# Performance work log

Hardware: AMD Instinct MI355X
Metric: run time of the kernel (lower is better)

The kernel has to match this reference:

```python
import jax, jax.numpy as jnp
import numpy as np
from math import sqrt

B, N, CS, H, D, K = 8, 256, 512, 8, 64, 32
NB = 2 * K + 1          # no_bins = 65
CT = 2048               # c_transition
INF = 1e9
WL = sqrt(0.5)          # w_L
EPS = 1e-5


def setup_inputs() -> dict:
    key = jax.random.key(0)
    ks = jax.random.split(key, 10)
    sc = 0.02
    return {
        "s": jax.random.normal(ks[0], (B, N, CS), jnp.float32),
        "masks": jnp.ones((B, N), jnp.bool_),
        "wq": jax.random.normal(ks[1], (CS, D * H), jnp.float32) * sc,
        "wk": jax.random.normal(ks[2], (CS, D * H), jnp.float32) * sc,
        "wv": jax.random.normal(ks[3], (CS, D * H), jnp.float32) * sc,
        "wb": jax.random.normal(ks[4], (NB, H), jnp.float32) * sc,
        "wo": jax.random.normal(ks[5], ((NB + D) * H, CS), jnp.float32) * sc,
        "bo": jnp.zeros((CS,), jnp.float32),
        "ln1_g": jnp.ones((CS,), jnp.float32),
        "ln1_b": jnp.zeros((CS,), jnp.float32),
        "w1": jax.random.normal(ks[6], (CS, CT), jnp.float32) * sc,
        "b1": jnp.zeros((CT,), jnp.float32),
        "w2": jax.random.normal(ks[7], (CT, CS), jnp.float32) * sc,
        "b2": jnp.zeros((CS,), jnp.float32),
        "ln2_g": jnp.ones((CS,), jnp.float32),
        "ln2_b": jnp.zeros((CS,), jnp.float32),
    }


def _layernorm(x, g, b):
    m = jnp.mean(x, -1, keepdims=True)
    v = jnp.var(x, -1, keepdims=True)
    return (x - m) * jax.lax.rsqrt(v + EPS) * g + b


def _heads(x):  # [B,N,D*H] -> [B,H,N,D]  (torch: reshape(B,N,D,H) then move H forward)
    return jnp.transpose(x.reshape(B, N, D, H), (0, 3, 1, 2))


def reference(s, masks, wq, wk, wv, wb, wo, bo, ln1_g, ln1_b, w1, b1, w2, b2, ln2_g, ln2_b):
    mf = masks.astype(s.dtype)                       # [B,N]
    sq = mf[:, :, None] * mf[:, None, :]             # [B,N,N]

    # relative position one-hot, clipped to [-K, K] -> [N,N,NB]
    r = jnp.arange(N)
    dmat = jnp.clip(r[:, None] - r[None, :], -K, K) + K
    relpos_base = jax.nn.one_hot(dmat, NB, dtype=s.dtype)
    relpos = relpos_base[None] * sq[..., None]       # [B,N,N,NB]

    b_bias = jnp.einsum('bijc,ch->bhij', relpos, wb)  # [B,H,N,N]

    q = _heads(s @ wq)                               # [B,H,N,D]
    k = _heads(s @ wk)
    v = _heads(s @ wv)

    logits = WL * (jnp.einsum('bhid,bhjd->bhij', q, k) / sqrt(D) + b_bias)
    logits = logits - INF * (1.0 - sq)[:, None]      # mask
    a = jax.nn.softmax(logits, axis=-1)              # [B,H,N,N]

    # pairwise aggregation and value aggregation (einsum avoids [B,H,N,N,NB] blowup)
    o_pair = jnp.einsum('bhij,bijc->bhic', a, relpos)  # [B,H,N,NB]
    o = jnp.einsum('bhij,bhjd->bhid', a, v)            # [B,H,N,D]

    op = jnp.transpose(o_pair, (0, 2, 1, 3)).reshape(B, N, H * NB)
    ov = jnp.transpose(o, (0, 2, 1, 3)).reshape(B, N, H * D)
    embd = jnp.concatenate([op, ov], axis=-1) @ wo + bo   # [B,N,CS]

    x = _layernorm(s + embd, ln1_g, ln1_b)
    ff = jax.nn.relu(x @ w1 + b1) @ w2 + b2
    x = _layernorm(x + ff, ln2_g, ln2_b)
    return x, a
```

## Files before the change

kernel.cpp:

```cpp
#include <hip/hip_runtime.h>
#include <hip/hip_bf16.h>
#include <cstdint>

#define B_ 8
#define N_ 256
#define CS_ 512
#define H_ 8
#define D_ 64
#define K_ 32
#define NB_ 65
#define CT_ 2048
#define WL_ 0.70710678118654752f

typedef __attribute__((ext_vector_type(8))) short bf16x8;
typedef __attribute__((ext_vector_type(4))) float f32x4;

#define GLOBAL_AS __attribute__((address_space(1)))
#define LDS_AS __attribute__((address_space(3)))

__device__ __forceinline__ void async16(void* lds, const void* g) {
  __builtin_amdgcn_global_load_lds((const GLOBAL_AS uint32_t*)g,
                                   (LDS_AS uint32_t*)lds, 16, 0, 0);
}

__device__ __forceinline__ ushort f2bf(float v) {
  __hip_bfloat16 hb = __float2bfloat16(v);
  return *(ushort*)&hb;
}

__device__ __forceinline__ float bf2f(ushort u) {
  union { uint32_t ui; float f; } cv; cv.ui = (uint32_t)u << 16;
  return cv.f;
}

__global__ __launch_bounds__(128, 2) void gemm_bf16(
    const ushort* __restrict__ A, const ushort* __restrict__ Bt,
    const float* __restrict__ bias, float* __restrict__ C,
    ushort* __restrict__ Cb, int M, int Nc, int Kd, int flags) {
  __shared__ ushort As[2][64 * 64];
  __shared__ ushort Bs[2][64 * 64];
  int tid = threadIdx.x;
  int bm = blockIdx.y * 64, bn = blockIdx.x * 64;
  int S = gridDim.z, z = blockIdx.z;
  int T = Kd >> 6;
  int it0 = (z * T) / S, it1 = ((z + 1) * T) / S;
  if (flags & 8)  C  += (size_t)z * M * Nc;
  if (flags & 32) Cb += (size_t)z * M * Nc;
  int w = tid >> 6, l = tid & 63;
  int lm = l & 15, lq = l >> 4;
  int srow = tid >> 3;
  int sg = tid & 7;

  f32x4 acc[2][4];
#pragma unroll
  for (int i = 0; i < 2; ++i)
#pragma unroll
    for (int j = 0; j < 4; ++j) acc[i][j] = (f32x4){0.f, 0.f, 0.f, 0.f};

  {
    int k0 = it0 << 6;
#pragma unroll
    for (int r = 0; r < 4; ++r) {
      int row = r * 16 + srow;
      int gl = sg ^ (row & 7);
      async16(&As[0][row * 64 + sg * 8],
              A + (size_t)(bm + row) * Kd + k0 + gl * 8);
      async16(&Bs[0][row * 64 + sg * 8],
              Bt + (size_t)(bn + row) * Kd + k0 + gl * 8);
    }
  }
  for (int it = it0; it < it1; ++it) {
    int cur = (it - it0) & 1;
    __syncthreads();
    if (it + 1 < it1) {
      int nxt = cur ^ 1;
      int k0 = (it + 1) << 6;
#pragma unroll
      for (int r = 0; r < 4; ++r) {
        int row = r * 16 + srow;
        int gl = sg ^ (row & 7);
        async16(&As[nxt][row * 64 + sg * 8],
                A + (size_t)(bm + row) * Kd + k0 + gl * 8);
        async16(&Bs[nxt][row * 64 + sg * 8],
                Bt + (size_t)(bn + row) * Kd + k0 + gl * 8);
      }
    }
#pragma unroll
    for (int kk = 0; kk < 2; ++kk) {
      bf16x8 af[2], bfr[4];
#pragma unroll
      for (int i = 0; i < 2; ++i) {
        int ma = w * 32 + 16 * i + lm;
        af[i] = *(const bf16x8*)&As[cur][ma * 64 + ((kk * 4 + lq) ^ (ma & 7)) * 8];
      }
#pragma unroll
      for (int j = 0; j < 4; ++j) {
        int nb = 16 * j + lm;
        bfr[j] = *(const bf16x8*)&Bs[cur][nb * 64 + ((kk * 4 + lq) ^ (nb & 7)) * 8];
      }
#pragma unroll
      for (int i = 0; i < 2; ++i)
#pragma unroll
        for (int j = 0; j < 4; ++j)
          acc[i][j] = __builtin_amdgcn_mfma_f32_16x16x32_bf16(
              af[i], bfr[j], acc[i][j], 0, 0, 0);
    }
  }
  __syncthreads();

  int lr = l >> 3, lc = l & 7;
  ushort* Tb = &As[0][0] + w * 2048;

  if (flags & 16) {
    int which = bn >> 9;
    int hh = (bn & 511) >> 6;
    int b = bm >> 8, nn0 = bm & 255;
    if (which == 2) {
#pragma unroll
      for (int j = 0; j < 4; ++j)
#pragma unroll
        for (int i = 0; i < 2; ++i) {
          ushort pk[4];
#pragma unroll
          for (int r = 0; r < 4; ++r) pk[r] = f2bf(acc[i][j][r]);
          *(uint2*)&Tb[(16 * j + lm) * 32 + 16 * i + lq * 4] = *(uint2*)pk;
        }
    } else {
#pragma unroll
      for (int j = 0; j < 4; ++j)
#pragma unroll
        for (int i = 0; i < 2; ++i)
#pragma unroll
          for (int r = 0; r < 4; ++r)
            Tb[(16 * i + lq * 4 + r) * 64 + 16 * j + lm] = f2bf(acc[i][j][r]);
    }
    __asm__ __volatile__("" ::: "memory");
    ushort* dstb = Cb + (size_t)which * 1048576 + (size_t)(b * 8 + hh) * 16384;
    if (which == 2) {
      int vr = l >> 2, vc = l & 3;
#pragma unroll
      for (int p = 0; p < 4; ++p) {
        int rowL = p * 16 + vr;
        bf16x8 vv = *(const bf16x8*)&Tb[rowL * 32 + vc * 8];
        *(bf16x8*)(dstb + (size_t)rowL * 256 + nn0 + w * 32 + vc * 8) = vv;
      }
    } else {
#pragma unroll
      for (int p = 0; p < 4; ++p) {
        int rowL = p * 8 + lr;
        bf16x8 vv = *(const bf16x8*)&Tb[rowL * 64 + lc * 8];
        *(bf16x8*)(dstb + (size_t)(nn0 + w * 32 + rowL) * 64 + lc * 8) = vv;
      }
    }
    return;
  }
  if (flags & 4) {
#pragma unroll
    for (int j = 0; j < 4; ++j) {
      float bv = ((flags & 1) && z == 0) ? bias[bn + 16 * j + lm] : 0.f;
#pragma unroll
      for (int i = 0; i < 2; ++i)
#pragma unroll
        for (int r = 0; r < 4; ++r) {
          float v = acc[i][j][r] + bv;
          if (flags & 2) v = fmaxf(v, 0.f);
          Tb[(16 * i + lq * 4 + r) * 64 + 16 * j + lm] = f2bf(v);
        }
    }
    __asm__ __volatile__("" ::: "memory");
#pragma unroll
    for (int p = 0; p < 4; ++p) {
      int rowL = p * 8 + lr;
      bf16x8 vv = *(const bf16x8*)&Tb[rowL * 64 + lc * 8];
      *(bf16x8*)(Cb + (size_t)(bm + w * 32 + rowL) * Nc + bn + lc * 8) = vv;
    }
    return;
  }
#pragma unroll
  for (int j = 0; j < 4; ++j) {
    int col = bn + 16 * j + lm;
    float bv = ((flags & 1) && z == 0) ? bias[col] : 0.f;
#pragma unroll
    for (int i = 0; i < 2; ++i)
#pragma unroll
      for (int r = 0; r < 4; ++r) {
        int row = bm + w * 32 + 16 * i + lq * 4 + r;
        float v = acc[i][j][r] + bv;
        if (flags & 2) v = fmaxf(v, 0.f);
        C[(size_t)row * Nc + col] = v;
      }
  }
}

__global__ __launch_bounds__(256) void prep_all(
    const float* __restrict__ s, __hip_bfloat16* __restrict__ s_bf,
    const float* __restrict__ wq, const float* __restrict__ wk,
    const float* __restrict__ wv, const float* __restrict__ wo,
    const float* __restrict__ w1, const float* __restrict__ w2,
    __hip_bfloat16* __restrict__ wqkvT, __hip_bfloat16* __restrict__ wopT,
    __hip_bfloat16* __restrict__ w1T, __hip_bfloat16* __restrict__ w2T) {
  int blk = blockIdx.x;
  if (blk < 512) {
    int i = blk * 256 + threadIdx.x;
    float4 a = ((const float4*)s)[i * 2];
    float4 c = ((const float4*)s)[i * 2 + 1];
    ushort pk[8] = {f2bf(a.x), f2bf(a.y), f2bf(a.z), f2bf(a.w),
                    f2bf(c.x), f2bf(c.y), f2bf(c.z), f2bf(c.w)};
    *(uint4*)&((ushort*)s_bf)[i * 8] = *(uint4*)pk;
    return;
  }
  blk -= 512;
  __shared__ float tile[32][33];
  const float* src;
  __hip_bfloat16* dst;
  int R, C, Kpad, tX, tIdx, whichBase = -1;
  if (blk < 768) {
    int zz = blk >> 8; tIdx = blk & 255;
    src = zz == 0 ? wq : zz == 1 ? wk : wv;
    dst = wqkvT; whichBase = zz * 512; R = 512; C = 512; Kpad = 512; tX = 16;
  } else if (blk < 1312) {
    tIdx = blk - 768; src = wo; dst = wopT; R = 1032; C = 512; Kpad = 1088; tX = 16;
  } else if (blk < 2336) {
    tIdx = blk - 1312; src = w1; dst = w1T; R = 512; C = 2048; Kpad = 512; tX = 64;
  } else {
    tIdx = blk - 2336; src = w2; dst = w2T; R = 2048; C = 512; Kpad = 2048; tX = 16;
  }
  int c0 = (tIdx % tX) * 32, r0 = (tIdx / tX) * 32;
  int tx = threadIdx.x & 31, ty = threadIdx.x >> 5;
#pragma unroll
  for (int yy = 0; yy < 32; yy += 8) {
    int r = r0 + ty + yy, c = c0 + tx;
    tile[ty + yy][tx] = (r < R && c < C) ? src[(size_t)r * C + c] : 0.f;
  }
  __syncthreads();
#pragma unroll
  for (int yy = 0; yy < 32; yy += 8) {
    int cc = c0 + ty + yy, k = r0 + tx;
    if (cc < C && k < Kpad) {
      int n = (whichBase >= 0) ? (whichBase + (cc & 7) * 64 + (cc >> 3)) : cc;
      dst[(size_t)n * Kpad + k] = __float2bfloat16(tile[tx][ty + yy]);
    }
  }
}

__global__ __launch_bounds__(128) void attn_fused(
    const ushort* __restrict__ qh, const ushort* __restrict__ kh,
    const ushort* __restrict__ vT, const int* __restrict__ masks,
    const float* __restrict__ wb, float* __restrict__ a_out,
    ushort* __restrict__ cat) {
  int strip = blockIdx.x & 7, bh = blockIdx.x >> 3;
  int h = bh & 7, b = bh >> 3;
  __shared__ ushort Ks[256 * 64];
  __shared__ ushort Ps[32 * 64];
  __shared__ float wbs[NB_];
  __shared__ float mfj[256];
  int tid = threadIdx.x;
  int srow = tid >> 3, sg = tid & 7;
#pragma unroll
  for (int rr = 0; rr < 16; ++rr) {
    int row = rr * 16 + srow;
    int gl = sg ^ (row & 7);
    async16(&Ks[row * 64 + sg * 8],
            kh + ((size_t)bh * 256 + row) * 64 + gl * 8);
  }
  int w = tid >> 6, l = tid & 63, lm = l & 15, lq = l >> 4;
  bf16x8 qf[2];
  {
    const ushort* qrow =
        qh + ((size_t)bh * 256 + strip * 32 + w * 16 + lm) * 64 + lq * 8;
    qf[0] = *(const bf16x8*)qrow;
    qf[1] = *(const bf16x8*)(qrow + 32);
  }
  if (tid < NB_) wbs[tid] = wb[tid * H_ + h];
  mfj[tid]       = (masks[b * 256 + tid] != 0) ? 1.f : 0.f;
  mfj[tid + 128] = (masks[b * 256 + tid + 128] != 0) ? 1.f : 0.f;
  __syncthreads();

  f32x4 acc[16];
#pragma unroll
  for (int ct = 0; ct < 16; ++ct) {
    int krow = ct * 16 + lm;
    bf16x8 kf0 = *(const bf16x8*)&Ks[krow * 64 + ((lq) ^ (krow & 7)) * 8];
    bf16x8 kf1 = *(const bf16x8*)&Ks[krow * 64 + ((4 + lq) ^ (krow & 7)) * 8];
    f32x4 zf = (f32x4){0.f, 0.f, 0.f, 0.f};
    zf = __builtin_amdgcn_mfma_f32_16x16x32_bf16(qf[0], kf0, zf, 0, 0, 0);
    acc[ct] = __builtin_amdgcn_mfma_f32_16x16x32_bf16(qf[1], kf1, zf, 0, 0, 0);
  }
  int ibase = strip * 32 + w * 16 + lq * 4;
  float mfi[4];
#pragma unroll
  for (int r = 0; r < 4; ++r) mfi[r] = mfj[ibase + r];
#pragma unroll
  for (int ct = 0; ct < 16; ++ct) {
    int j = ct * 16 + lm;
    float mj = mfj[j];
#pragma unroll
    for (int r = 0; r < 4; ++r) {
      int i = ibase + r;
      int diff = i - j;
      int cb = diff < -K_ ? 0 : (diff > K_ ? 2 * K_ : diff + K_);
      float sq = mfi[r] * mj;
      acc[ct][r] = WL_ * (acc[ct][r] * 0.125f + wbs[cb] * sq) - 1e9f * (1.f - sq);
    }
  }
  float mx[4], sm[4];
#pragma unroll
  for (int r = 0; r < 4; ++r) {
    float m = acc[0][r];
#pragma unroll
    for (int ct = 1; ct < 16; ++ct) m = fmaxf(m, acc[ct][r]);
#pragma unroll
    for (int o = 1; o < 16; o <<= 1) m = fmaxf(m, __shfl_xor(m, o, 64));
    mx[r] = m;
  }
#pragma unroll
  for (int ct = 0; ct < 16; ++ct)
#pragma unroll
    for (int r = 0; r < 4; ++r) acc[ct][r] = __expf(acc[ct][r] - mx[r]);
#pragma unroll
  for (int r = 0; r < 4; ++r) {
    float s = 0.f;
#pragma unroll
    for (int ct = 0; ct < 16; ++ct) s += acc[ct][r];
#pragma unroll
    for (int o = 1; o < 16; o <<= 1) s += __shfl_xor(s, o, 64);
    sm[r] = 1.f / s;
  }
  float p0[4] = {0.f, 0.f, 0.f, 0.f}, p64[4] = {0.f, 0.f, 0.f, 0.f};
#pragma unroll
  for (int ct = 0; ct < 16; ++ct) {
    int j = ct * 16 + lm;
    float mj = mfj[j];
#pragma unroll
    for (int r = 0; r < 4; ++r) {
      int i = ibase + r;
      float aval = acc[ct][r] * sm[r];
      a_out[((size_t)bh * 256 + i) * 256 + j] = aval;
      float val = aval * mfi[r] * mj;
      int diff = i - j;
      if (diff <= -K_)      p0[r] += val;
      else if (diff >= K_)  p64[r] += val;
      else cat[((size_t)(b * 256 + i)) * 1088 + h * 65 + diff + K_] = f2bf(val);
    }
  }
#pragma unroll
  for (int r = 0; r < 4; ++r)
#pragma unroll
    for (int o = 1; o < 16; o <<= 1) {
      p0[r]  += __shfl_xor(p0[r], o, 64);
      p64[r] += __shfl_xor(p64[r], o, 64);
    }
  if (lm == 0) {
#pragma unroll
    for (int r = 0; r < 4; ++r) {
      int i = ibase + r;
      cat[((size_t)(b * 256 + i)) * 1088 + h * 65 + 0]      = f2bf(p0[r]);
      cat[((size_t)(b * 256 + i)) * 1088 + h * 65 + 2 * K_] = f2bf(p64[r]);
    }
  }
#pragma unroll
  for (int r = 0; r < 4; ++r) {
    int i = ibase + r;
#pragma unroll
    for (int t = 0; t < 4; ++t) {
      int c = 1 + lm + 16 * t;
      if (c < 64) {
        int j = i - c + K_;
        if (j < 0 || j > 255)
          cat[((size_t)(b * 256 + i)) * 1088 + h * 65 + c] = 0;
      }
    }
  }
  if (h == 0) {
    for (int idx = tid; idx < 32 * 56; idx += 128) {
      int r = idx / 56, c = 1032 + (idx - r * 56);
      cat[((size_t)(b * 256 + strip * 32 + r)) * 1088 + c] = 0;
    }
  }
  f32x4 acc2[4];
#pragma unroll
  for (int nt = 0; nt < 4; ++nt) acc2[nt] = (f32x4){0.f, 0.f, 0.f, 0.f};
  const ushort* vbase = vT + (size_t)bh * 16384;
#pragma unroll
  for (int qt = 0; qt < 4; ++qt) {
    bf16x8 vf0[4], vf1[4];
#pragma unroll
    for (int nt = 0; nt < 4; ++nt) {
      const ushort* vrow = vbase + (size_t)(nt * 16 + lm) * 256 + qt * 64 + lq * 8;
      vf0[nt] = *(const bf16x8*)vrow;
      vf1[nt] = *(const bf16x8*)(vrow + 32);
    }
#pragma unroll
    for (int ctl = 0; ctl < 4; ++ctl) {
      int ct = qt * 4 + ctl;
#pragma unroll
      for (int r = 0; r < 4; ++r) {
        int rowl = w * 16 + lq * 4 + r;
        int g = ctl * 2 + (lm >> 3);
        Ps[rowl * 64 + ((g ^ (rowl & 7)) << 3) + (lm & 7)] =
            f2bf(acc[ct][r] * sm[r]);
      }
    }
    int prow = w * 16 + lm;
#pragma unroll
    for (int kst = 0; kst < 2; ++kst) {
      bf16x8 af = *(const bf16x8*)&Ps[prow * 64 + (((kst * 4 + lq) ^ (prow & 7)) << 3)];
#pragma unroll
      for (int nt = 0; nt < 4; ++nt)
        acc2[nt] = __builtin_amdgcn_mfma_f32_16x16x32_bf16(
            af, kst ? vf1[nt] : vf0[nt], acc2[nt], 0, 0, 0);
    }
  }
#pragma unroll
  for (int nt = 0; nt < 4; ++nt) {
    int d = nt * 16 + lm;
#pragma unroll
    for (int r = 0; r < 4; ++r) {
      int i = ibase + r;
      cat[((size_t)(b * 256 + i)) * 1088 + 520 + h * 64 + d] = f2bf(acc2[nt][r]);
    }
  }
}

__global__ __launch_bounds__(128) void ln_sum(
    const float* __restrict__ x1, const ushort* __restrict__ xp,
    int S, int stride, const float* __restrict__ g,
    const float* __restrict__ bta, float* __restrict__ out,
    __hip_bfloat16* __restrict__ out_bf) {
  __shared__ float redA[2], redB[2];
  int row = blockIdx.x, tid = threadIdx.x;
  size_t base = (size_t)row * 512;
  float4 v = *(const float4*)(x1 + base + tid * 4);
  for (int s = 0; s < S; ++s) {
    uint2 p = *(const uint2*)(xp + (size_t)s * stride + base + tid * 4);
    v.x += bf2f((ushort)(p.x & 0xffff));
    v.y += bf2f((ushort)(p.x >> 16));
    v.z += bf2f((ushort)(p.y & 0xffff));
    v.w += bf2f((ushort)(p.y >> 16));
  }
  float su = v.x + v.y + v.z + v.w;
  float sq = v.x * v.x + v.y * v.y + v.z * v.z + v.w * v.w;
#pragma unroll
  for (int o = 32; o > 0; o >>= 1) {
    su += __shfl_xor(su, o, 64);
    sq += __shfl_xor(sq, o, 64);
  }
  int w = tid >> 6;
  if ((tid & 63) == 0) { redA[w] = su; redB[w] = sq; }
  __syncthreads();
  su = redA[0] + redA[1]; sq = redB[0] + redB[1];
  float mean = su * (1.f / 512.f);
  float var = sq * (1.f / 512.f) - mean * mean;
  float inv = rsqrtf(var + 1e-5f);
  float4 gv = *(const float4*)(g + tid * 4);
  float4 bv = *(const float4*)(bta + tid * 4);
  float4 o4;
  o4.x = (v.x - mean) * inv * gv.x + bv.x;
  o4.y = (v.y - mean) * inv * gv.y + bv.y;
  o4.z = (v.z - mean) * inv * gv.z + bv.z;
  o4.w = (v.w - mean) * inv * gv.w + bv.w;
  *(float4*)(out + base + tid * 4) = o4;
  if (out_bf) {
    ushort pk[4] = {f2bf(o4.x), f2bf(o4.y), f2bf(o4.z), f2bf(o4.w)};
    *(uint2*)&((ushort*)out_bf)[base + tid * 4] = *(uint2*)pk;
  }
}

extern "C" void kernel_launch(void* const* d_in, const int* in_sizes, int n_in,
                              void* d_out, int out_size, void* d_ws, size_t ws_size,
                              hipStream_t stream) {
  const float* s     = (const float*)d_in[0];
  const int*   masks = (const int*)d_in[1];
  const float* wq = (const float*)d_in[2];
  const float* wk = (const float*)d_in[3];
  const float* wv = (const float*)d_in[4];
  const float* wb = (const float*)d_in[5];
  const float* wo = (const float*)d_in[6];
  const float* bo = (const float*)d_in[7];
  const float* ln1_g = (const float*)d_in[8];
  const float* ln1_b = (const float*)d_in[9];
  const float* w1 = (const float*)d_in[10];
  const float* b1 = (const float*)d_in[11];
  const float* w2 = (const float*)d_in[12];
  const float* b2 = (const float*)d_in[13];
  const float* ln2_g = (const float*)d_in[14];
  const float* ln2_b = (const float*)d_in[15];

  float* out_x = (float*)d_out;
  float* out_a = out_x + 1048576;

  float* ws = (float*)d_ws;
  ushort* embd_part = (ushort*)(ws + 0);
  float* xbuf       = ws + 4194304;
  ushort* ff_part   = (ushort*)(ws + 5242880);
  ushort* qkv_bf    = (ushort*)(ws + 9437184);
  ushort* q_bf = qkv_bf;
  ushort* k_bf = qkv_bf + 1048576;
  ushort* v_bf = qkv_bf + 2097152;
  ushort* cat_bf = (ushort*)(ws + 10223616);
  __hip_bfloat16* h_bf  = (__hip_bfloat16*)(ws + 11337728);
  __hip_bfloat16* s_bf  = (__hip_bfloat16*)(ws + 13434880);
  __hip_bfloat16* x_bf  = (__hip_bfloat16*)(ws + 13959168);
  __hip_bfloat16* wqkvT = (__hip_bfloat16*)(ws + 14483456);
  __hip_bfloat16* wopT  = (__hip_bfloat16*)(ws + 14876672);
  __hip_bfloat16* w1T   = (__hip_bfloat16*)(ws + 15155200);
  __hip_bfloat16* w2T   = (__hip_bfloat16*)(ws + 15679488);

  dim3 blk(256), blkg(128);
  prep_all<<<dim3(3872), blk, 0, stream>>>(s, s_bf, wq, wk, wv, wo, w1, w2,
                                           wqkvT, wopT, w1T, w2T);
  gemm_bf16<<<dim3(24, 32, 1), blkg, 0, stream>>>(
      (const ushort*)s_bf, (const ushort*)wqkvT, nullptr, nullptr,
      qkv_bf, 2048, 1536, 512, 16);
  attn_fused<<<dim3(512), blkg, 0, stream>>>(q_bf, k_bf, v_bf, masks, wb,
                                             out_a, cat_bf);
  gemm_bf16<<<dim3(8, 32, 4), blkg, 0, stream>>>(
      cat_bf, (const ushort*)wopT, bo, nullptr, embd_part,
      2048, 512, 1088, 1 | 4 | 32);
  ln_sum<<<dim3(2048), blkg, 0, stream>>>(s, embd_part, 4, 1048576,
                                          ln1_g, ln1_b, xbuf, x_bf);
  gemm_bf16<<<dim3(32, 32, 1), blkg, 0, stream>>>(
      (const ushort*)x_bf, (const ushort*)w1T, b1, nullptr, (ushort*)h_bf,
      2048, 2048, 512, 1 | 2 | 4);
  gemm_bf16<<<dim3(8, 32, 4), blkg, 0, stream>>>(
      (const ushort*)h_bf, (const ushort*)w2T, b2, nullptr, ff_part,
      2048, 512, 2048, 1 | 4 | 32);
  ln_sum<<<dim3(2048), blkg, 0, stream>>>(xbuf, ff_part, 4, 1048576,
                                          ln2_g, ln2_b, out_x, nullptr);
}
```

Measured before the change: 172.4 us.

## Overlap wo/w1/w2 weight transposition with QKV GEMM and halve split-K

Splits the preprocessing so only s and the QKV weights are converted up front. The wo/w1/w2 transposes are folded into extra blocks of a new QKV GEMM kernel, so they run alongside the projection instead of before it. The transposes now use float4 loads and packed bf16 stores. Split-K for the output and FFN2 GEMMs drops from 4 to 2, which halves the partial buffers that ln_sum reduces but gives fewer blocks to hide latency.

```diff
diff --git a/kernel.cpp b/kernel.cpp
--- a/kernel.cpp
+++ b/kernel.cpp
@@ -44,7 +44,6 @@
   int S = gridDim.z, z = blockIdx.z;
   int T = Kd >> 6;
   int it0 = (z * T) / S, it1 = ((z + 1) * T) / S;
-  if (flags & 8)  C  += (size_t)z * M * Nc;
   if (flags & 32) Cb += (size_t)z * M * Nc;
   int w = tid >> 6, l = tid & 63;
   int lm = l & 15, lq = l >> 4;
@@ -111,94 +110,184 @@
   int lr = l >> 3, lc = l & 7;
   ushort* Tb = &As[0][0] + w * 2048;
 
-  if (flags & 16) {
-    int which = bn >> 9;
-    int hh = (bn & 511) >> 6;
-    int b = bm >> 8, nn0 = bm & 255;
-    if (which == 2) {
-#pragma unroll
-      for (int j = 0; j < 4; ++j)
-#pragma unroll
-        for (int i = 0; i < 2; ++i) {
-          ushort pk[4];
-#pragma unroll
-          for (int r = 0; r < 4; ++r) pk[r] = f2bf(acc[i][j][r]);
-          *(uint2*)&Tb[(16 * j + lm) * 32 + 16 * i + lq * 4] = *(uint2*)pk;
-        }
-    } else {
-#pragma unroll
-      for (int j = 0; j < 4; ++j)
-#pragma unroll
-        for (int i = 0; i < 2; ++i)
-#pragma unroll
-          for (int r = 0; r < 4; ++r)
-            Tb[(16 * i + lq * 4 + r) * 64 + 16 * j + lm] = f2bf(acc[i][j][r]);
-    }
-    __asm__ __volatile__("" ::: "memory");
-    ushort* dstb = Cb + (size_t)which * 1048576 + (size_t)(b * 8 + hh) * 16384;
-    if (which == 2) {
-      int vr = l >> 2, vc = l & 3;
-#pragma unroll
-      for (int p = 0; p < 4; ++p) {
-        int rowL = p * 16 + vr;
-        bf16x8 vv = *(const bf16x8*)&Tb[rowL * 32 + vc * 8];
-        *(bf16x8*)(dstb + (size_t)rowL * 256 + nn0 + w * 32 + vc * 8) = vv;
-      }
-    } else {
-#pragma unroll
-      for (int p = 0; p < 4; ++p) {
-        int rowL = p * 8 + lr;
-        bf16x8 vv = *(const bf16x8*)&Tb[rowL * 64 + lc * 8];
-        *(bf16x8*)(dstb + (size_t)(nn0 + w * 32 + rowL) * 64 + lc * 8) = vv;
-      }
+#pragma unroll
+  for (int j = 0; j < 4; ++j) {
+    float bv = ((flags & 1) && z == 0) ? bias[bn + 16 * j + lm] : 0.f;
+#pragma unroll
+    for (int i = 0; i < 2; ++i)
+#pragma unroll
+      for (int r = 0; r < 4; ++r) {
+        float v = acc[i][j][r] + bv;
+        if (flags & 2) v = fmaxf(v, 0.f);
+        Tb[(16 * i + lq * 4 + r) * 64 + 16 * j + lm] = f2bf(v);
+      }
+  }
+  __asm__ __volatile__("" ::: "memory");
+#pragma unroll
+  for (int p = 0; p < 4; ++p) {
+    int rowL = p * 8 + lr;
+    bf16x8 vv = *(const bf16x8*)&Tb[rowL * 64 + lc * 8];
+    *(bf16x8*)(Cb + (size_t)(bm + w * 32 + rowL) * Nc + bn + lc * 8) = vv;
+  }
+}
+
+__global__ __launch_bounds__(128, 2) void qkvT(
+    const ushort* __restrict__ A, const ushort* __restrict__ Bt,
+    ushort* __restrict__ Cb,
+    const float* __restrict__ wo, const float* __restrict__ w1,
+    const float* __restrict__ w2, ushort* __restrict__ wopT,
+    ushort* __restrict__ w1T, ushort* __restrict__ w2T) {
+  __shared__ __align__(16) ushort As[2][64 * 64];
+  __shared__ ushort Bs[2][64 * 64];
+  int blk = blockIdx.x, tid = threadIdx.x;
+
+  if (blk >= 768) {
+    float (*tile)[33] = (float(*)[33])&As[0][0];
+    int t = blk - 768;
+    const float* src; ushort* dst;
+    int R, C, Kpad, tX, tIdx;
+    if (t < 544)       { tIdx = t;        src = wo; dst = wopT; R = 1032; C = 512;  Kpad = 1088; tX = 16; }
+    else if (t < 1568) { tIdx = t - 544;  src = w1; dst = w1T;  R = 512;  C = 2048; Kpad = 512;  tX = 64; }
+    else               { tIdx = t - 1568; src = w2; dst = w2T;  R = 2048; C = 512;  Kpad = 2048; tX = 16; }
+    int c0 = (tIdx % tX) * 32, r0 = (tIdx / tX) * 32;
+    int tx = tid & 7, ty = tid >> 3;
+#pragma unroll
+    for (int yy = 0; yy < 32; yy += 16) {
+      int r = r0 + yy + ty, c = c0 + tx * 4;
+      float4 v = (r < R) ? *(const float4*)&src[(size_t)r * C + c]
+                         : (float4){0.f, 0.f, 0.f, 0.f};
+      tile[yy + ty][tx * 4 + 0] = v.x;
+      tile[yy + ty][tx * 4 + 1] = v.y;
+      tile[yy + ty][tx * 4 + 2] = v.z;
+      tile[yy + ty][tx * 4 + 3] = v.w;
+    }
+    __syncthreads();
+#pragma unroll
+    for (int yy = 0; yy < 32; yy += 16) {
+      int cc = c0 + yy + ty;
+      int k = r0 + tx * 4;
+      float a0 = tile[tx * 4 + 0][yy + ty];
+      float a1 = tile[tx * 4 + 1][yy + ty];
+      float a2 = tile[tx * 4 + 2][yy + ty];
+      float a3 = tile[tx * 4 + 3][yy + ty];
+      ushort pk[4] = {f2bf(a0), f2bf(a1), f2bf(a2), f2bf(a3)};
+      *(uint2*)&dst[(size_t)cc * Kpad + k] = *(uint2*)pk;
     }
     return;
   }
-  if (flags & 4) {
-#pragma unroll
-    for (int j = 0; j < 4; ++j) {
-      float bv = ((flags & 1) && z == 0) ? bias[bn + 16 * j + lm] : 0.f;
+
+  int bm = (blk / 24) * 64, bn = (blk % 24) * 64;
+  const int Kd = 512, it1 = 8;
+  int w = tid >> 6, l = tid & 63;
+  int lm = l & 15, lq = l >> 4;
+  int srow = tid >> 3;
+  int sg = tid & 7;
+
+  f32x4 acc[2][4];
+#pragma unroll
+  for (int i = 0; i < 2; ++i)
+#pragma unroll
+    for (int j = 0; j < 4; ++j) acc[i][j] = (f32x4){0.f, 0.f, 0.f, 0.f};
+
+  {
+#pragma unroll
+    for (int r = 0; r < 4; ++r) {
+      int row = r * 16 + srow;
+      int gl = sg ^ (row & 7);
+      async16(&As[0][row * 64 + sg * 8],
+              A + (size_t)(bm + row) * Kd + gl * 8);
+      async16(&Bs[0][row * 64 + sg * 8],
+              Bt + (size_t)(bn + row) * Kd + gl * 8);
+    }
+  }
+  for (int it = 0; it < it1; ++it) {
+    int cur = it & 1;
+    __syncthreads();
+    if (it + 1 < it1) {
+      int nxt = cur ^ 1;
+      int k0 = (it + 1) << 6;
+#pragma unroll
+      for (int r = 0; r < 4; ++r) {
+        int row = r * 16 + srow;
+        int gl = sg ^ (row & 7);
+        async16(&As[nxt][row * 64 + sg * 8],
+                A + (size_t)(bm + row) * Kd + k0 + gl * 8);
+        async16(&Bs[nxt][row * 64 + sg * 8],
+                Bt + (size_t)(bn + row) * Kd + k0 + gl * 8);
+      }
+    }
+#pragma unroll
+    for (int kk = 0; kk < 2; ++kk) {
+      bf16x8 af[2], bfr[4];
+#pragma unroll
+      for (int i = 0; i < 2; ++i) {
+        int ma = w * 32 + 16 * i + lm;
+        af[i] = *(const bf16x8*)&As[cur][ma * 64 + ((kk * 4 + lq) ^ (ma & 7)) * 8];
+      }
+#pragma unroll
+      for (int j = 0; j < 4; ++j) {
+        int nb = 16 * j + lm;
+        bfr[j] = *(const bf16x8*)&Bs[cur][nb * 64 + ((kk * 4 + lq) ^ (nb & 7)) * 8];
+      }
 #pragma unroll
       for (int i = 0; i < 2; ++i)
 #pragma unroll
-        for (int r = 0; r < 4; ++r) {
-          float v = acc[i][j][r] + bv;
-          if (flags & 2) v = fmaxf(v, 0.f);
-          Tb[(16 * i + lq * 4 + r) * 64 + 16 * j + lm] = f2bf(v);
-        }
-    }
-    __asm__ __volatile__("" ::: "memory");
+        for (int j = 0; j < 4; ++j)
+          acc[i][j] = __builtin_amdgcn_mfma_f32_16x16x32_bf16(
+              af[i], bfr[j], acc[i][j], 0, 0, 0);
+    }
+  }
+  __syncthreads();
+
+  int lr = l >> 3, lc = l & 7;
+  ushort* Tb = &As[0][0] + w * 2048;
+
+  int which = bn >> 9;
+  int hh = (bn & 511) >> 6;
+  int b = bm >> 8, nn0 = bm & 255;
+  if (which == 2) {
+#pragma unroll
+    for (int j = 0; j < 4; ++j)
+#pragma unroll
+      for (int i = 0; i < 2; ++i) {
+        ushort pk[4];
+#pragma unroll
+        for (int r = 0; r < 4; ++r) pk[r] = f2bf(acc[i][j][r]);
+        *(uint2*)&Tb[(16 * j + lm) * 32 + 16 * i + lq * 4] = *(uint2*)pk;
+      }
+  } else {
+#pragma unroll
+    for (int j = 0; j < 4; ++j)
+#pragma unroll
+      for (int i = 0; i < 2; ++i)
+#pragma unroll
+        for (int r = 0; r < 4; ++r)
+          Tb[(16 * i + lq * 4 + r) * 64 + 16 * j + lm] = f2bf(acc[i][j][r]);
+  }
+  __asm__ __volatile__("" ::: "memory");
+  ushort* dstb = Cb + (size_t)which * 1048576 + (size_t)(b * 8 + hh) * 16384;
+  if (which == 2) {
+    int vr = l >> 2, vc = l & 3;
+#pragma unroll
+    for (int p = 0; p < 4; ++p) {
+      int rowL = p * 16 + vr;
+      bf16x8 vv = *(const bf16x8*)&Tb[rowL * 32 + vc * 8];
+      *(bf16x8*)(dstb + (size_t)rowL * 256 + nn0 + w * 32 + vc * 8) = vv;
+    }
+  } else {
 #pragma unroll
     for (int p = 0; p < 4; ++p) {
       int rowL = p * 8 + lr;
       bf16x8 vv = *(const bf16x8*)&Tb[rowL * 64 + lc * 8];
-      *(bf16x8*)(Cb + (size_t)(bm + w * 32 + rowL) * Nc + bn + lc * 8) = vv;
-    }
-    return;
-  }
-#pragma unroll
-  for (int j = 0; j < 4; ++j) {
-    int col = bn + 16 * j + lm;
-    float bv = ((flags & 1) && z == 0) ? bias[col] : 0.f;
-#pragma unroll
-    for (int i = 0; i < 2; ++i)
-#pragma unroll
-      for (int r = 0; r < 4; ++r) {
-        int row = bm + w * 32 + 16 * i + lq * 4 + r;
-        float v = acc[i][j][r] + bv;
-        if (flags & 2) v = fmaxf(v, 0.f);
-        C[(size_t)row * Nc + col] = v;
-      }
-  }
-}
-
-__global__ __launch_bounds__(256) void prep_all(
+      *(bf16x8*)(dstb + (size_t)(nn0 + w * 32 + rowL) * 64 + lc * 8) = vv;
+    }
+  }
+}
+
+__global__ __launch_bounds__(256) void prep_small(
     const float* __restrict__ s, __hip_bfloat16* __restrict__ s_bf,
     const float* __restrict__ wq, const float* __restrict__ wk,
-    const float* __restrict__ wv, const float* __restrict__ wo,
-    const float* __restrict__ w1, const float* __restrict__ w2,
-    __hip_bfloat16* __restrict__ wqkvT, __hip_bfloat16* __restrict__ wopT,
-    __hip_bfloat16* __restrict__ w1T, __hip_bfloat16* __restrict__ w2T) {
+    const float* __restrict__ wv, __hip_bfloat16* __restrict__ wqkvT) {
   int blk = blockIdx.x;
   if (blk < 512) {
     int i = blk * 256 + threadIdx.x;
@@ -209,37 +298,32 @@
     *(uint4*)&((ushort*)s_bf)[i * 8] = *(uint4*)pk;
     return;
   }
-  blk -= 512;
+  int t = blk - 512;
   __shared__ float tile[32][33];
-  const float* src;
-  __hip_bfloat16* dst;
-  int R, C, Kpad, tX, tIdx, whichBase = -1;
-  if (blk < 768) {
-    int zz = blk >> 8; tIdx = blk & 255;
-    src = zz == 0 ? wq : zz == 1 ? wk : wv;
-    dst = wqkvT; whichBase = zz * 512; R = 512; C = 512; Kpad = 512; tX = 16;
-  } else if (blk < 1312) {
-    tIdx = blk - 768; src = wo; dst = wopT; R = 1032; C = 512; Kpad = 1088; tX = 16;
-  } else if (blk < 2336) {
-    tIdx = blk - 1312; src = w1; dst = w1T; R = 512; C = 2048; Kpad = 512; tX = 64;
-  } else {
-    tIdx = blk - 2336; src = w2; dst = w2T; R = 2048; C = 512; Kpad = 2048; tX = 16;
-  }
-  int c0 = (tIdx % tX) * 32, r0 = (tIdx / tX) * 32;
-  int tx = threadIdx.x & 31, ty = threadIdx.x >> 5;
-#pragma unroll
-  for (int yy = 0; yy < 32; yy += 8) {
-    int r = r0 + ty + yy, c = c0 + tx;
-    tile[ty + yy][tx] = (r < R && c < C) ? src[(size_t)r * C + c] : 0.f;
+  int zz = t >> 8, tIdx = t & 255;
+  const float* src = zz == 0 ? wq : zz == 1 ? wk : wv;
+  int whichBase = zz * 512;
+  int c0 = (tIdx & 15) * 32, r0 = (tIdx >> 4) * 32;
+  int tx = threadIdx.x & 7, ty = threadIdx.x >> 3;
+  {
+    int r = r0 + ty, c = c0 + tx * 4;
+    float4 v = *(const float4*)&src[(size_t)r * 512 + c];
+    tile[ty][tx * 4 + 0] = v.x;
+    tile[ty][tx * 4 + 1] = v.y;
+    tile[ty][tx * 4 + 2] = v.z;
+    tile[ty][tx * 4 + 3] = v.w;
   }
   __syncthreads();
-#pragma unroll
-  for (int yy = 0; yy < 32; yy += 8) {
-    int cc = c0 + ty + yy, k = r0 + tx;
-    if (cc < C && k < Kpad) {
-      int n = (whichBase >= 0) ? (whichBase + (cc & 7) * 64 + (cc >> 3)) : cc;
-      dst[(size_t)n * Kpad + k] = __float2bfloat16(tile[tx][ty + yy]);
-    }
+  {
+    int cc = c0 + ty;
+    int k = r0 + tx * 4;
+    float a0 = tile[tx * 4 + 0][ty];
+    float a1 = tile[tx * 4 + 1][ty];
+    float a2 = tile[tx * 4 + 2][ty];
+    float a3 = tile[tx * 4 + 3][ty];
+    int n = whichBase + (cc & 7) * 64 + (cc >> 3);
+    ushort pk[4] = {f2bf(a0), f2bf(a1), f2bf(a2), f2bf(a3)};
+    *(uint2*)&((ushort*)wqkvT)[(size_t)n * 512 + k] = *(uint2*)pk;
   }
 }
 
@@ -502,29 +586,27 @@
   __hip_bfloat16* s_bf  = (__hip_bfloat16*)(ws + 13434880);
   __hip_bfloat16* x_bf  = (__hip_bfloat16*)(ws + 13959168);
   __hip_bfloat16* wqkvT = (__hip_bfloat16*)(ws + 14483456);
-  __hip_bfloat16* wopT  = (__hip_bfloat16*)(ws + 14876672);
-  __hip_bfloat16* w1T   = (__hip_bfloat16*)(ws + 15155200);
-  __hip_bfloat16* w2T   = (__hip_bfloat16*)(ws + 15679488);
-
-  dim3 blk(256), blkg(128);
-  prep_all<<<dim3(3872), blk, 0, stream>>>(s, s_bf, wq, wk, wv, wo, w1, w2,
-                                           wqkvT, wopT, w1T, w2T);
-  gemm_bf16<<<dim3(24, 32, 1), blkg, 0, stream>>>(
-      (const ushort*)s_bf, (const ushort*)wqkvT, nullptr, nullptr,
-      qkv_bf, 2048, 1536, 512, 16);
+  ushort* wopT  = (ushort*)(ws + 14876672);
+  ushort* w1T   = (ushort*)(ws + 15155200);
+  ushort* w2T   = (ushort*)(ws + 15679488);
+
+  dim3 blkg(128);
+  prep_small<<<dim3(1280), dim3(256), 0, stream>>>(s, s_bf, wq, wk, wv, wqkvT);
+  qkvT<<<dim3(3360), blkg, 0, stream>>>(
+      (const ushort*)s_bf, (const ushort*)wqkvT, qkv_bf,
+      wo, w1, w2, wopT, w1T, w2T);
   attn_fused<<<dim3(512), blkg, 0, stream>>>(q_bf, k_bf, v_bf, masks, wb,
                                              out_a, cat_bf);
-  gemm_bf16<<<dim3(8, 32, 4), blkg, 0, stream>>>(
-      cat_bf, (const ushort*)wopT, bo, nullptr, embd_part,
-      2048, 512, 1088, 1 | 4 | 32);
-  ln_sum<<<dim3(2048), blkg, 0, stream>>>(s, embd_part, 4, 1048576,
+  gemm_bf16<<<dim3(8, 32, 2), blkg, 0, stream>>>(
+      cat_bf, wopT, bo, nullptr, embd_part, 2048, 512, 1088, 1 | 4 | 32);
+  ln_sum<<<dim3(2048), blkg, 0, stream>>>(s, embd_part, 2, 1048576,
                                           ln1_g, ln1_b, xbuf, x_bf);
   gemm_bf16<<<dim3(32, 32, 1), blkg, 0, stream>>>(
-      (const ushort*)x_bf, (const ushort*)w1T, b1, nullptr, (ushort*)h_bf,
+      (const ushort*)x_bf, w1T, b1, nullptr, (ushort*)h_bf,
       2048, 2048, 512, 1 | 2 | 4);
-  gemm_bf16<<<dim3(8, 32, 4), blkg, 0, stream>>>(
-      (const ushort*)h_bf, (const ushort*)w2T, b2, nullptr, ff_part,
+  gemm_bf16<<<dim3(8, 32, 2), blkg, 0, stream>>>(
+      (const ushort*)h_bf, w2T, b2, nullptr, ff_part,
       2048, 512, 2048, 1 | 4 | 32);
-  ln_sum<<<dim3(2048), blkg, 0, stream>>>(xbuf, ff_part, 4, 1048576,
+  ln_sum<<<dim3(2048), blkg, 0, stream>>>(xbuf, ff_part, 2, 1048576,
                                           ln2_g, ln2_b, out_x, nullptr);
 }
```

Measured after the change: 169.3 us, median of 2. Within noise of the previous version (-1.8%).
